# Optimization experiments

Hardware: AMD Instinct MI355X
Metric: run time of the kernel (lower is better)

## Reference

```python
import jax, jax.numpy as jnp
import numpy as np

H = 16  # num_attention_heads

def setup_inputs() -> dict:
    key = jax.random.key(0)
    ks = jax.random.split(key, 9)
    D = 1152
    def w(k, shape, scale=0.02):
        return jax.random.normal(k, shape, dtype=jnp.float32) * scale
    return {
        "hidden_states": jax.random.normal(ks[0], (16, 729, D), dtype=jnp.float32),
        "q_w": w(ks[1], (D, D)), "q_b": w(ks[2], (D,)),
        "k_w": w(ks[3], (D, D)), "k_b": w(ks[4], (D,)),
        "v_w": w(ks[5], (D, D)), "v_b": w(ks[6], (D,)),
        "o_w": w(ks[7], (D, D)), "o_b": w(ks[8], (D,)),
    }

def reference(hidden_states, q_w, q_b, k_w, k_b, v_w, v_b, o_w, o_b):
    B, S, D = hidden_states.shape
    hd = D // H
    scale = hd ** -0.5
    # projections (torch Linear: x @ W.T + b)
    q = hidden_states @ q_w.T + q_b
    k = hidden_states @ k_w.T + k_b
    v = hidden_states @ v_w.T + v_b
    # [B, H, S, hd]
    q = q.reshape(B, S, H, hd).transpose(0, 2, 1, 3)
    k = k.reshape(B, S, H, hd).transpose(0, 2, 1, 3)
    v = v.reshape(B, S, H, hd).transpose(0, 2, 1, 3)
    scores = jnp.einsum('bhqd,bhkd->bhqk', q, k) * scale
    attn = jax.nn.softmax(scores.astype(jnp.float32), axis=-1).astype(q.dtype)
    # dropout p=0.0 / eval mode -> identity
    out = jnp.einsum('bhqk,bhkd->bhqd', attn, v)  # [B,H,S,hd]
    out = out.transpose(0, 2, 1, 3).reshape(B, S, D)
    out = out @ o_w.T + o_b
    return (out, attn)
```

## Files before the change

kernel.cpp:

```cpp
#include <hip/hip_runtime.h>
#include <cstdint>
#include <cstddef>

typedef _Float16 half8 __attribute__((ext_vector_type(8)));
typedef _Float16 half4 __attribute__((ext_vector_type(4)));
typedef float    f32x4 __attribute__((ext_vector_type(4)));
typedef float    fvec4 __attribute__((ext_vector_type(4)));

#define DEV __device__ __forceinline__

constexpr int S_  = 729;
constexpr int D_  = 1152;
constexpr int H_  = 16;
constexpr int HD_ = 72;
constexpr int B_  = 16;
constexpr int M1  = B_ * S_;
constexpr int SP  = 768;
constexpr int HDP = 96;
constexpr int QSTR = 104;
constexpr float SCALE = 0.11785113019775793f;

DEV void gload16(const void* g, void* l) {
  typedef const __attribute__((address_space(1))) unsigned int GU;
  typedef __attribute__((address_space(3))) unsigned int LU;
  __builtin_amdgcn_global_load_lds((GU*)g, (LU*)l, 16, 0, 0);
}

__global__ void cvt_f32_f16(const float* __restrict__ src, _Float16* __restrict__ dst, int n4) {
  int stride = gridDim.x * blockDim.x;
  for (int i = blockIdx.x * blockDim.x + threadIdx.x; i < n4; i += stride) {
    fvec4 v = ((const fvec4*)src)[i];
    half4 o;
    o[0] = (_Float16)v[0]; o[1] = (_Float16)v[1];
    o[2] = (_Float16)v[2]; o[3] = (_Float16)v[3];
    ((half4*)dst)[i] = o;
  }
}

__global__ __launch_bounds__(256) void gemm_qkv(
    const _Float16* __restrict__ A, const _Float16* __restrict__ W,
    const float* __restrict__ qb, const float* __restrict__ kb, const float* __restrict__ vb,
    _Float16* __restrict__ q16, _Float16* __restrict__ k16, _Float16* __restrict__ vT16)
{
  __shared__ _Float16 lA[128 * 32];
  __shared__ _Float16 lB[128 * 32];
  const int tid  = threadIdx.x;
  const int wave = tid >> 6, lane = tid & 63;
  const int wr = wave >> 1, wc = wave & 1;
  const int l15 = lane & 15, l4 = lane >> 4;
  const int rowBase = blockIdx.y * 128;
  const int colBase = blockIdx.x * 128;

  f32x4 acc[4][4] = {};

  for (int kt = 0; kt < 36; ++kt) {
#pragma unroll
    for (int p = 0; p < 2; ++p) {
      int u = p * 256 + tid;
      int r = u >> 2, q = u & 3;
      int row = rowBase + r; if (row > M1 - 1) row = M1 - 1;
      gload16(A + ((size_t)row * 1152 + kt * 32 + q * 8), &lA[u * 8]);
      gload16(W + ((size_t)(colBase + r) * 1152 + kt * 32 + q * 8), &lB[u * 8]);
    }
    __syncthreads();
    half8 af[4], bf[4];
#pragma unroll
    for (int i = 0; i < 4; ++i) {
      af[i] = *(const half8*)&lA[(wr * 64 + i * 16 + l15) * 32 + l4 * 8];
      bf[i] = *(const half8*)&lB[(wc * 64 + i * 16 + l15) * 32 + l4 * 8];
    }
#pragma unroll
    for (int mi = 0; mi < 4; ++mi)
#pragma unroll
      for (int ni = 0; ni < 4; ++ni)
        acc[mi][ni] = __builtin_amdgcn_mfma_f32_16x16x32_f16(af[mi], bf[ni], acc[mi][ni], 0, 0, 0);
    __syncthreads();
  }

  const int which = colBase / 1152;
  const int wi0 = colBase - which * 1152 + wc * 64;
  const float* bias = (which == 0) ? qb : (which == 1) ? kb : vb;
#pragma unroll
  for (int ni = 0; ni < 4; ++ni) {
    int wi = wi0 + ni * 16 + l15;
    int hh = wi / 72;
    int dd = wi - hh * 72;
    float bv = bias[wi];
#pragma unroll
    for (int mi = 0; mi < 4; ++mi) {
#pragma unroll
      for (int reg = 0; reg < 4; ++reg) {
        int m = rowBase + wr * 64 + mi * 16 + l4 * 4 + reg;
        if (m < M1) {
          float val = acc[mi][ni][reg] + bv;
          int b = m / 729;
          int s = m - b * 729;
          int bh = b * 16 + hh;
          if (which == 0)      q16[((size_t)bh * SP + s) * QSTR + dd] = (_Float16)val;
          else if (which == 1) k16[((size_t)bh * SP + s) * QSTR + dd] = (_Float16)val;
          else                 vT16[((size_t)bh * HDP + dd) * SP + s] = (_Float16)val;
        }
      }
    }
  }
}

__global__ __launch_bounds__(256) void attn_fused(
    const _Float16* __restrict__ q16, const _Float16* __restrict__ k16,
    const _Float16* __restrict__ vT16,
    float* __restrict__ attnOut,
    _Float16* __restrict__ pv16)
{
  __shared__ _Float16 sQ[32 * QSTR];
  __shared__ _Float16 sK[128 * QSTR];
  __shared__ float    sS[32 * 772];
  __shared__ float    sM[32];
  __shared__ float    sL[32];

  const int tid  = threadIdx.x;
  const int wave = tid >> 6, lane = tid & 63;
  const int l15 = lane & 15, l4 = lane >> 4;
  const int rb = blockIdx.x;
  const int bh = blockIdx.y;

  const _Float16* Qg = q16 + ((size_t)bh * SP + rb * 32) * QSTR;
  const _Float16* Kg = k16 + (size_t)bh * SP * QSTR;
  const _Float16* Vg = vT16 + (size_t)bh * HDP * SP;

  for (int u = tid; u < 416; u += 256)
    gload16((const char*)Qg + u * 16, (char*)sQ + u * 16);

  for (int ct = 0; ct < 6; ++ct) {
    for (int u = tid; u < 1664; u += 256)
      gload16((const char*)Kg + (size_t)ct * 128 * QSTR * 2 + u * 16, (char*)sK + u * 16);
    __syncthreads();
    f32x4 acc[2][2] = {};
#pragma unroll
    for (int kk = 0; kk < 3; ++kk) {
      half8 a[2], bb[2];
#pragma unroll
      for (int i = 0; i < 2; ++i) {
        a[i]  = *(const half8*)&sQ[(i * 16 + l15) * QSTR + kk * 32 + l4 * 8];
        bb[i] = *(const half8*)&sK[(wave * 32 + i * 16 + l15) * QSTR + kk * 32 + l4 * 8];
      }
#pragma unroll
      for (int mi = 0; mi < 2; ++mi)
#pragma unroll
        for (int ni = 0; ni < 2; ++ni)
          acc[mi][ni] = __builtin_amdgcn_mfma_f32_16x16x32_f16(a[mi], bb[ni], acc[mi][ni], 0, 0, 0);
    }
#pragma unroll
    for (int mi = 0; mi < 2; ++mi)
#pragma unroll
      for (int ni = 0; ni < 2; ++ni)
#pragma unroll
        for (int reg = 0; reg < 4; ++reg)
          sS[(mi * 16 + l4 * 4 + reg) * 772 + ct * 128 + wave * 32 + ni * 16 + l15] =
              acc[mi][ni][reg] * SCALE;
    __syncthreads();
  }

  {
    int r = tid >> 3, j = tid & 7;
    const float* row = &sS[r * 772];
    float mx = -1e30f;
    for (int c = j; c < S_; c += 8) mx = fmaxf(mx, row[c]);
#pragma unroll
    for (int o = 1; o < 8; o <<= 1) mx = fmaxf(mx, __shfl_xor(mx, o));
    float sum = 0.f;
    for (int c = j; c < S_; c += 8) sum += __expf(row[c] - mx);
#pragma unroll
    for (int o = 1; o < 8; o <<= 1) sum += __shfl_xor(sum, o);
    if (j == 0) { sM[r] = mx; sL[r] = 1.0f / sum; }
  }
  __syncthreads();

  {
    const int wm = wave >> 1, wn = wave & 1;
    const int arow = wm * 16 + l15;
    const float mrow = sM[arow];
    const float rl = sL[arow];
    f32x4 pacc[3] = {};
    for (int kk = 0; kk < 24; ++kk) {
      const float* sp = &sS[arow * 772 + kk * 32 + l4 * 8];
      half8 a;
#pragma unroll
      for (int t = 0; t < 8; ++t) a[t] = (_Float16)(__expf(sp[t] - mrow) * rl);
#pragma unroll
      for (int f = 0; f < 3; ++f) {
        const half8 bv = *(const half8*)(Vg + (size_t)(wn * 48 + f * 16 + l15) * SP + kk * 32 + l4 * 8);
        pacc[f] = __builtin_amdgcn_mfma_f32_16x16x32_f16(a, bv, pacc[f], 0, 0, 0);
      }
    }
    const int b = bh >> 4, h = bh & 15;
#pragma unroll
    for (int f = 0; f < 3; ++f) {
      int dd = wn * 48 + f * 16 + l15;
#pragma unroll
      for (int reg = 0; reg < 4; ++reg) {
        int srow = rb * 32 + wm * 16 + l4 * 4 + reg;
        if (dd < HD_ && srow < S_)
          pv16[((size_t)(b * 729 + srow)) * 1152 + h * 72 + dd] = (_Float16)pacc[f][reg];
      }
    }
  }

  {
    float* aout = attnOut + (size_t)bh * 531441 + (size_t)rb * 32 * 729;
    int vr = S_ - rb * 32; if (vr > 32) vr = 32;
    for (int r = 0; r < vr; ++r) {
      float mx = sM[r], rl = sL[r];
      const float* row = &sS[r * 772];
      for (int c = tid; c < S_; c += 256)
        aout[(size_t)r * 729 + c] = __expf(row[c] - mx) * rl;
    }
  }
}

__global__ __launch_bounds__(256) void gemm_out(
    const _Float16* __restrict__ A, const _Float16* __restrict__ W,
    const float* __restrict__ ob, float* __restrict__ Cout)
{
  __shared__ _Float16 lA[128 * 32];
  __shared__ _Float16 lB[128 * 32];
  const int tid  = threadIdx.x;
  const int wave = tid >> 6, lane = tid & 63;
  const int wr = wave >> 1, wc = wave & 1;
  const int l15 = lane & 15, l4 = lane >> 4;
  const int rowBase = blockIdx.y * 128;
  const int colBase = blockIdx.x * 128;

  f32x4 acc[4][4] = {};

  for (int kt = 0; kt < 36; ++kt) {
#pragma unroll
    for (int p = 0; p < 2; ++p) {
      int u = p * 256 + tid;
      int r = u >> 2, q = u & 3;
      int row = rowBase + r; if (row > M1 - 1) row = M1 - 1;
      gload16(A + ((size_t)row * 1152 + kt * 32 + q * 8), &lA[u * 8]);
      gload16(W + ((size_t)(colBase + r) * 1152 + kt * 32 + q * 8), &lB[u * 8]);
    }
    __syncthreads();
    half8 af[4], bf[4];
#pragma unroll
    for (int i = 0; i < 4; ++i) {
      af[i] = *(const half8*)&lA[(wr * 64 + i * 16 + l15) * 32 + l4 * 8];
      bf[i] = *(const half8*)&lB[(wc * 64 + i * 16 + l15) * 32 + l4 * 8];
    }
#pragma unroll
    for (int mi = 0; mi < 4; ++mi)
#pragma unroll
      for (int ni = 0; ni < 4; ++ni)
        acc[mi][ni] = __builtin_amdgcn_mfma_f32_16x16x32_f16(af[mi], bf[ni], acc[mi][ni], 0, 0, 0);
    __syncthreads();
  }

#pragma unroll
  for (int ni = 0; ni < 4; ++ni) {
    int n = colBase + wc * 64 + ni * 16 + l15;
    float bv = ob[n];
#pragma unroll
    for (int mi = 0; mi < 4; ++mi) {
#pragma unroll
      for (int reg = 0; reg < 4; ++reg) {
        int m = rowBase + wr * 64 + mi * 16 + l4 * 4 + reg;
        if (m < M1) Cout[(size_t)m * 1152 + n] = acc[mi][ni][reg] + bv;
      }
    }
  }
}

extern "C" void kernel_launch(void* const* d_in, const int* in_sizes, int n_in,
                              void* d_out, int out_size, void* d_ws, size_t ws_size,
                              hipStream_t stream) {
  const float* hs = (const float*)d_in[0];
  const float* qw = (const float*)d_in[1];
  const float* qb = (const float*)d_in[2];
  const float* kw = (const float*)d_in[3];
  const float* kb = (const float*)d_in[4];
  const float* vw = (const float*)d_in[5];
  const float* vb = (const float*)d_in[6];
  const float* ow = (const float*)d_in[7];
  const float* ob = (const float*)d_in[8];

  char* ws = (char*)d_ws;
  size_t off = 0;
  auto alloc = [&](size_t bytes) {
    char* p = ws + off;
    off = (off + bytes + 255) & ~(size_t)255;
    return p;
  };
  _Float16* h16    = (_Float16*)alloc((size_t)M1 * D_ * 2);
  _Float16* wqkv16 = (_Float16*)alloc((size_t)3456 * 1152 * 2);
  _Float16* ow16   = (_Float16*)alloc((size_t)1152 * 1152 * 2);
  _Float16* q16    = (_Float16*)alloc((size_t)256 * SP * QSTR * 2);
  _Float16* k16    = (_Float16*)alloc((size_t)256 * SP * QSTR * 2);
  _Float16* vT16   = (_Float16*)alloc((size_t)256 * HDP * SP * 2);
  _Float16* pv16   = (_Float16*)alloc((size_t)M1 * D_ * 2);

  hipMemsetAsync(q16,  0, (size_t)256 * SP * QSTR * 2, stream);
  hipMemsetAsync(k16,  0, (size_t)256 * SP * QSTR * 2, stream);
  hipMemsetAsync(vT16, 0, (size_t)256 * HDP * SP * 2, stream);

  cvt_f32_f16<<<2048, 256, 0, stream>>>(hs, h16, M1 * D_ / 4);
  cvt_f32_f16<<<512, 256, 0, stream>>>(qw, wqkv16,                 1152 * 1152 / 4);
  cvt_f32_f16<<<512, 256, 0, stream>>>(kw, wqkv16 + 1152 * 1152,   1152 * 1152 / 4);
  cvt_f32_f16<<<512, 256, 0, stream>>>(vw, wqkv16 + 2 * 1152 * 1152, 1152 * 1152 / 4);
  cvt_f32_f16<<<512, 256, 0, stream>>>(ow, ow16, 1152 * 1152 / 4);

  gemm_qkv<<<dim3(27, 92), 256, 0, stream>>>(h16, wqkv16, qb, kb, vb, q16, k16, vT16);

  float* attn_out = (float*)d_out + (size_t)M1 * D_;
  attn_fused<<<dim3(23, 256), 256, 0, stream>>>(q16, k16, vT16, attn_out, pv16);

  gemm_out<<<dim3(9, 92), 256, 0, stream>>>(pv16, ow16, ob, (float*)d_out);
}
```

Before: 1.566 ms.

## Double-buffer K tiles, widen attention block to 512 threads, store exps once

The attention kernel moves to 512 threads per block and double-buffers K tiles in LDS, using manual vmcnt waits and raw barriers so the next tile's load overlaps the current QK^T MFMAs. Softmax exponentials are computed once and written back into the score buffer. The attention-probability output is written with vectorized float4 stores, and the 1/sum normalization is deferred to the PV output. The PV product is split across two K halves with an LDS reduction, and block indices are swizzled for better locality. The hand-tuned waitcnt counts and extra LDS raise the risk of correctness problems and of lower occupancy.

```diff
diff --git a/kernel.cpp b/kernel.cpp
--- a/kernel.cpp
+++ b/kernel.cpp
@@ -5,6 +5,7 @@
 typedef _Float16 half8 __attribute__((ext_vector_type(8)));
 typedef _Float16 half4 __attribute__((ext_vector_type(4)));
 typedef float    f32x4 __attribute__((ext_vector_type(4)));
+typedef float    f32x4_u __attribute__((ext_vector_type(4), aligned(4)));
 typedef float    fvec4 __attribute__((ext_vector_type(4)));
 
 #define DEV __device__ __forceinline__
@@ -25,6 +26,8 @@
   typedef __attribute__((address_space(3))) unsigned int LU;
   __builtin_amdgcn_global_load_lds((GU*)g, (LU*)l, 16, 0, 0);
 }
+
+DEV void fence_mem() { asm volatile("" ::: "memory"); }
 
 __global__ void cvt_f32_f16(const float* __restrict__ src, _Float16* __restrict__ dst, int n4) {
   int stride = gridDim.x * blockDim.x;
@@ -105,114 +108,150 @@
   }
 }
 
-__global__ __launch_bounds__(256) void attn_fused(
+DEV void stageK(const _Float16* src, _Float16* dst, int wv, int lane) {
+  for (int c = wv; c < 26; c += 8)
+    gload16((const char*)src + c * 1024 + lane * 16, (char*)dst + c * 1024 + lane * 16);
+}
+
+__global__ __launch_bounds__(512) void attn_fused(
     const _Float16* __restrict__ q16, const _Float16* __restrict__ k16,
     const _Float16* __restrict__ vT16,
     float* __restrict__ attnOut,
     _Float16* __restrict__ pv16)
 {
-  __shared__ _Float16 sQ[32 * QSTR];
-  __shared__ _Float16 sK[128 * QSTR];
-  __shared__ float    sS[32 * 772];
-  __shared__ float    sM[32];
-  __shared__ float    sL[32];
+  __shared__ __align__(16) _Float16 sQ[32 * QSTR];
+  __shared__ __align__(16) _Float16 sKb[2][128 * QSTR];
+  __shared__ __align__(16) float    sS[32 * 772];
+  __shared__ float sL[32];
+  float* red = (float*)&sKb[0][0];
 
   const int tid  = threadIdx.x;
-  const int wave = tid >> 6, lane = tid & 63;
-  const int l15 = lane & 15, l4 = lane >> 4;
-  const int rb = blockIdx.x;
-  const int bh = blockIdx.y;
+  const int wv   = tid >> 6, lane = tid & 63;
+  const int l15  = lane & 15, l4 = lane >> 4;
+
+  const int lin  = blockIdx.y * 23 + blockIdx.x;
+  const int nlin = (lin & 7) * 736 + (lin >> 3);
+  const int bh   = nlin / 23;
+  const int rb   = nlin - bh * 23;
 
   const _Float16* Qg = q16 + ((size_t)bh * SP + rb * 32) * QSTR;
   const _Float16* Kg = k16 + (size_t)bh * SP * QSTR;
   const _Float16* Vg = vT16 + (size_t)bh * HDP * SP;
 
-  for (int u = tid; u < 416; u += 256)
-    gload16((const char*)Qg + u * 16, (char*)sQ + u * 16);
+  if (tid < 416) {
+    half8 v = *(const half8*)(Qg + tid * 8);
+    *(half8*)(sQ + tid * 8) = v;
+  }
+  stageK(Kg, sKb[0], wv, lane);
+  __syncthreads();
 
   for (int ct = 0; ct < 6; ++ct) {
-    for (int u = tid; u < 1664; u += 256)
-      gload16((const char*)Kg + (size_t)ct * 128 * QSTR * 2 + u * 16, (char*)sK + u * 16);
-    __syncthreads();
-    f32x4 acc[2][2] = {};
+    const _Float16* cur = sKb[ct & 1];
+    if (ct < 5) {
+      stageK(Kg + (ct + 1) * (128 * QSTR), sKb[(ct + 1) & 1], wv, lane);
+      if (wv < 2) asm volatile("s_waitcnt vmcnt(4)" ::: "memory");
+      else        asm volatile("s_waitcnt vmcnt(3)" ::: "memory");
+    } else {
+      asm volatile("s_waitcnt vmcnt(0)" ::: "memory");
+    }
+    __builtin_amdgcn_s_barrier();
+    fence_mem();
+
+    f32x4 acc0 = {0.f, 0.f, 0.f, 0.f};
+    f32x4 acc1 = {0.f, 0.f, 0.f, 0.f};
 #pragma unroll
     for (int kk = 0; kk < 3; ++kk) {
-      half8 a[2], bb[2];
-#pragma unroll
-      for (int i = 0; i < 2; ++i) {
-        a[i]  = *(const half8*)&sQ[(i * 16 + l15) * QSTR + kk * 32 + l4 * 8];
-        bb[i] = *(const half8*)&sK[(wave * 32 + i * 16 + l15) * QSTR + kk * 32 + l4 * 8];
+      half8 a0 = *(const half8*)&sQ[(l15) * QSTR + kk * 32 + l4 * 8];
+      half8 a1 = *(const half8*)&sQ[(16 + l15) * QSTR + kk * 32 + l4 * 8];
+      half8 b  = *(const half8*)&cur[(wv * 16 + l15) * QSTR + kk * 32 + l4 * 8];
+      acc0 = __builtin_amdgcn_mfma_f32_16x16x32_f16(a0, b, acc0, 0, 0, 0);
+      acc1 = __builtin_amdgcn_mfma_f32_16x16x32_f16(a1, b, acc1, 0, 0, 0);
+    }
+#pragma unroll
+    for (int r = 0; r < 4; ++r) {
+      sS[(l4 * 4 + r) * 772 + ct * 128 + wv * 16 + l15]        = acc0[r] * SCALE;
+      sS[(16 + l4 * 4 + r) * 772 + ct * 128 + wv * 16 + l15]   = acc1[r] * SCALE;
+    }
+    asm volatile("s_waitcnt lgkmcnt(0)" ::: "memory");
+    __builtin_amdgcn_s_barrier();
+    fence_mem();
+  }
+
+  const int sr = tid >> 4, sj = tid & 15;
+  float m = -1e30f;
+  for (int c = sj; c < 729; c += 16) m = fmaxf(m, sS[sr * 772 + c]);
+#pragma unroll
+  for (int o = 1; o < 16; o <<= 1) m = fmaxf(m, __shfl_xor(m, o));
+  float sum = 0.f;
+  for (int c = sj; c < 768; c += 16) {
+    float s = sS[sr * 772 + c];
+    float e = (c < 729) ? __expf(s - m) : 0.f;
+    sS[sr * 772 + c] = e;
+    sum += e;
+  }
+#pragma unroll
+  for (int o = 1; o < 16; o <<= 1) sum += __shfl_xor(sum, o);
+  const float rl = 1.0f / sum;
+  if (sj == 0) sL[sr] = rl;
+  __syncthreads();
+
+  {
+    const int grow = rb * 32 + sr;
+    float* aout = attnOut + (size_t)bh * 531441 + (size_t)grow * 729;
+    if (grow < 729) {
+#pragma unroll
+      for (int it = 0; it < 12; ++it) {
+        int c4 = sj + it * 16;
+        if (c4 < 182) {
+          f32x4 e = *(const f32x4*)&sS[sr * 772 + c4 * 4];
+          f32x4 p = e * rl;
+          *(f32x4_u*)&aout[c4 * 4] = p;
+        }
       }
-#pragma unroll
-      for (int mi = 0; mi < 2; ++mi)
-#pragma unroll
-        for (int ni = 0; ni < 2; ++ni)
-          acc[mi][ni] = __builtin_amdgcn_mfma_f32_16x16x32_f16(a[mi], bb[ni], acc[mi][ni], 0, 0, 0);
-    }
-#pragma unroll
-    for (int mi = 0; mi < 2; ++mi)
-#pragma unroll
-      for (int ni = 0; ni < 2; ++ni)
-#pragma unroll
-        for (int reg = 0; reg < 4; ++reg)
-          sS[(mi * 16 + l4 * 4 + reg) * 772 + ct * 128 + wave * 32 + ni * 16 + l15] =
-              acc[mi][ni][reg] * SCALE;
-    __syncthreads();
-  }
-
-  {
-    int r = tid >> 3, j = tid & 7;
-    const float* row = &sS[r * 772];
-    float mx = -1e30f;
-    for (int c = j; c < S_; c += 8) mx = fmaxf(mx, row[c]);
-#pragma unroll
-    for (int o = 1; o < 8; o <<= 1) mx = fmaxf(mx, __shfl_xor(mx, o));
-    float sum = 0.f;
-    for (int c = j; c < S_; c += 8) sum += __expf(row[c] - mx);
-#pragma unroll
-    for (int o = 1; o < 8; o <<= 1) sum += __shfl_xor(sum, o);
-    if (j == 0) { sM[r] = mx; sL[r] = 1.0f / sum; }
+      if (sj == 6) aout[728] = sS[sr * 772 + 728] * rl;
+    }
+  }
+
+  const int wm = wv >> 2, wn = (wv >> 1) & 1, kh = wv & 1;
+  f32x4 pacc[3] = {};
+  const _Float16* Vw = Vg + (size_t)wn * 48 * SP;
+  for (int kk = kh * 12; kk < kh * 12 + 12; ++kk) {
+    const float* sp = &sS[(wm * 16 + l15) * 772 + kk * 32 + l4 * 8];
+    f32x4 e0 = *(const f32x4*)sp;
+    f32x4 e1 = *(const f32x4*)(sp + 4);
+    half8 a;
+    a[0] = (_Float16)e0[0]; a[1] = (_Float16)e0[1];
+    a[2] = (_Float16)e0[2]; a[3] = (_Float16)e0[3];
+    a[4] = (_Float16)e1[0]; a[5] = (_Float16)e1[1];
+    a[6] = (_Float16)e1[2]; a[7] = (_Float16)e1[3];
+#pragma unroll
+    for (int f = 0; f < 3; ++f) {
+      half8 bv = *(const half8*)&Vw[(size_t)(f * 16 + l15) * SP + kk * 32 + l4 * 8];
+      pacc[f] = __builtin_amdgcn_mfma_f32_16x16x32_f16(a, bv, pacc[f], 0, 0, 0);
+    }
+  }
+  const int unit = wv >> 1;
+  if (kh == 1) {
+#pragma unroll
+    for (int f = 0; f < 3; ++f)
+      *(f32x4*)&red[((unit * 3 + f) * 64 + lane) * 4] = pacc[f];
   }
   __syncthreads();
-
-  {
-    const int wm = wave >> 1, wn = wave & 1;
-    const int arow = wm * 16 + l15;
-    const float mrow = sM[arow];
-    const float rl = sL[arow];
-    f32x4 pacc[3] = {};
-    for (int kk = 0; kk < 24; ++kk) {
-      const float* sp = &sS[arow * 772 + kk * 32 + l4 * 8];
-      half8 a;
-#pragma unroll
-      for (int t = 0; t < 8; ++t) a[t] = (_Float16)(__expf(sp[t] - mrow) * rl);
-#pragma unroll
-      for (int f = 0; f < 3; ++f) {
-        const half8 bv = *(const half8*)(Vg + (size_t)(wn * 48 + f * 16 + l15) * SP + kk * 32 + l4 * 8);
-        pacc[f] = __builtin_amdgcn_mfma_f32_16x16x32_f16(a, bv, pacc[f], 0, 0, 0);
+  if (kh == 0) {
+    const int b = bh >> 4, h = bh & 15;
+#pragma unroll
+    for (int f = 0; f < 3; ++f) {
+      f32x4 o = pacc[f] + *(const f32x4*)&red[((unit * 3 + f) * 64 + lane) * 4];
+      int dd = wn * 48 + f * 16 + l15;
+#pragma unroll
+      for (int r = 0; r < 4; ++r) {
+        int row  = wm * 16 + l4 * 4 + r;
+        int srow = rb * 32 + row;
+        if (dd < HD_ && srow < S_) {
+          float val = o[r] * sL[row];
+          pv16[((size_t)(b * 729 + srow)) * 1152 + h * 72 + dd] = (_Float16)val;
+        }
       }
-    }
-    const int b = bh >> 4, h = bh & 15;
-#pragma unroll
-    for (int f = 0; f < 3; ++f) {
-      int dd = wn * 48 + f * 16 + l15;
-#pragma unroll
-      for (int reg = 0; reg < 4; ++reg) {
-        int srow = rb * 32 + wm * 16 + l4 * 4 + reg;
-        if (dd < HD_ && srow < S_)
-          pv16[((size_t)(b * 729 + srow)) * 1152 + h * 72 + dd] = (_Float16)pacc[f][reg];
-      }
-    }
-  }
-
-  {
-    float* aout = attnOut + (size_t)bh * 531441 + (size_t)rb * 32 * 729;
-    int vr = S_ - rb * 32; if (vr > 32) vr = 32;
-    for (int r = 0; r < vr; ++r) {
-      float mx = sM[r], rl = sL[r];
-      const float* row = &sS[r * 772];
-      for (int c = tid; c < S_; c += 256)
-        aout[(size_t)r * 729 + c] = __expf(row[c] - mx) * rl;
     }
   }
 }
@@ -304,15 +343,15 @@
   hipMemsetAsync(vT16, 0, (size_t)256 * HDP * SP * 2, stream);
 
   cvt_f32_f16<<<2048, 256, 0, stream>>>(hs, h16, M1 * D_ / 4);
-  cvt_f32_f16<<<512, 256, 0, stream>>>(qw, wqkv16,                 1152 * 1152 / 4);
-  cvt_f32_f16<<<512, 256, 0, stream>>>(kw, wqkv16 + 1152 * 1152,   1152 * 1152 / 4);
+  cvt_f32_f16<<<512, 256, 0, stream>>>(qw, wqkv16,                   1152 * 1152 / 4);
+  cvt_f32_f16<<<512, 256, 0, stream>>>(kw, wqkv16 + 1152 * 1152,     1152 * 1152 / 4);
   cvt_f32_f16<<<512, 256, 0, stream>>>(vw, wqkv16 + 2 * 1152 * 1152, 1152 * 1152 / 4);
   cvt_f32_f16<<<512, 256, 0, stream>>>(ow, ow16, 1152 * 1152 / 4);
 
   gemm_qkv<<<dim3(27, 92), 256, 0, stream>>>(h16, wqkv16, qb, kb, vb, q16, k16, vT16);
 
   float* attn_out = (float*)d_out + (size_t)M1 * D_;
-  attn_fused<<<dim3(23, 256), 256, 0, stream>>>(q16, k16, vT16, attn_out, pv16);
+  attn_fused<<<dim3(23, 256), 512, 0, stream>>>(q16, k16, vT16, attn_out, pv16);
 
   gemm_out<<<dim3(9, 92), 256, 0, stream>>>(pv16, ow16, ob, (float*)d_out);
 }
```

New measurement: 1.373 ms. 12.3% less time.

## Rewrite attention kernel to keep scores in registers with split-K softmax

Applied to the files above, without the earlier changes.

The attention kernel now processes 16 query rows per block. Each of the four waves owns a 192-key slice and keeps its scores in registers, so the large LDS score buffer is gone. Per-wave max and sum statistics are combined through a small LDS exchange, probabilities are written straight to the attention output with vector stores, and the PV products from each wave are reduced through LDS. A swizzled block index and launch bounds aimed at higher occupancy are added. In exchange it relies on heavy register use for the score tiles, switches to the smaller 16x16x16 MFMA for PV, and leaves the final normalization to the end.

```diff
diff --git a/kernel.cpp b/kernel.cpp
--- a/kernel.cpp
+++ b/kernel.cpp
@@ -5,6 +5,7 @@
 typedef _Float16 half8 __attribute__((ext_vector_type(8)));
 typedef _Float16 half4 __attribute__((ext_vector_type(4)));
 typedef float    f32x4 __attribute__((ext_vector_type(4)));
+typedef float    f32x4_u __attribute__((ext_vector_type(4), aligned(4)));
 typedef float    fvec4 __attribute__((ext_vector_type(4)));
 
 #define DEV __device__ __forceinline__
@@ -105,114 +106,131 @@
   }
 }
 
-__global__ __launch_bounds__(256) void attn_fused(
+__global__ __launch_bounds__(256, 4) void attn_fused(
     const _Float16* __restrict__ q16, const _Float16* __restrict__ k16,
     const _Float16* __restrict__ vT16,
     float* __restrict__ attnOut,
     _Float16* __restrict__ pv16)
 {
-  __shared__ _Float16 sQ[32 * QSTR];
-  __shared__ _Float16 sK[128 * QSTR];
-  __shared__ float    sS[32 * 772];
-  __shared__ float    sM[32];
-  __shared__ float    sL[32];
+  __shared__ __align__(16) float sRed[3][16][80];
+  __shared__ float sStat[4][16][2];
 
   const int tid  = threadIdx.x;
-  const int wave = tid >> 6, lane = tid & 63;
-  const int l15 = lane & 15, l4 = lane >> 4;
-  const int rb = blockIdx.x;
-  const int bh = blockIdx.y;
-
-  const _Float16* Qg = q16 + ((size_t)bh * SP + rb * 32) * QSTR;
-  const _Float16* Kg = k16 + (size_t)bh * SP * QSTR;
-  const _Float16* Vg = vT16 + (size_t)bh * HDP * SP;
-
-  for (int u = tid; u < 416; u += 256)
-    gload16((const char*)Qg + u * 16, (char*)sQ + u * 16);
-
-  for (int ct = 0; ct < 6; ++ct) {
-    for (int u = tid; u < 1664; u += 256)
-      gload16((const char*)Kg + (size_t)ct * 128 * QSTR * 2 + u * 16, (char*)sK + u * 16);
-    __syncthreads();
-    f32x4 acc[2][2] = {};
-#pragma unroll
-    for (int kk = 0; kk < 3; ++kk) {
-      half8 a[2], bb[2];
-#pragma unroll
-      for (int i = 0; i < 2; ++i) {
-        a[i]  = *(const half8*)&sQ[(i * 16 + l15) * QSTR + kk * 32 + l4 * 8];
-        bb[i] = *(const half8*)&sK[(wave * 32 + i * 16 + l15) * QSTR + kk * 32 + l4 * 8];
+  const int wv   = tid >> 6, lane = tid & 63;
+  const int l15  = lane & 15, l4 = lane >> 4;
+
+  const int lin  = blockIdx.y * 48 + blockIdx.x;
+  const int nlin = (lin & 7) * 1536 + (lin >> 3);
+  const int bh   = nlin / 48;
+  const int rb   = nlin - bh * 48;
+  const int q0   = rb * 16;
+
+  const _Float16* Qg = q16 + ((size_t)bh * SP + q0) * QSTR;
+  const _Float16* Kg = k16 + ((size_t)bh * SP + wv * 192) * QSTR;
+  const _Float16* Vg = vT16 + (size_t)bh * HDP * SP + wv * 192;
+
+  half8 qf[3];
+#pragma unroll
+  for (int d = 0; d < 3; ++d)
+    qf[d] = *(const half8*)(Qg + (size_t)l15 * QSTR + d * 32 + l4 * 8);
+
+  float sc[12][4];
+  float m_ln = -1e30f;
+#pragma unroll
+  for (int t = 0; t < 12; ++t) {
+    f32x4 a = {0.f, 0.f, 0.f, 0.f};
+#pragma unroll
+    for (int d = 0; d < 3; ++d) {
+      half8 kf = *(const half8*)(Kg + (size_t)(t * 16 + l15) * QSTR + d * 32 + l4 * 8);
+      a = __builtin_amdgcn_mfma_f32_16x16x32_f16(kf, qf[d], a, 0, 0, 0);
+    }
+#pragma unroll
+    for (int r = 0; r < 4; ++r) {
+      int kidx = wv * 192 + t * 16 + l4 * 4 + r;
+      float s = (kidx < S_) ? a[r] * SCALE : -1e30f;
+      sc[t][r] = s;
+      m_ln = fmaxf(m_ln, s);
+    }
+  }
+  float l_ln = 0.f;
+#pragma unroll
+  for (int t = 0; t < 12; ++t)
+#pragma unroll
+    for (int r = 0; r < 4; ++r) l_ln += __expf(sc[t][r] - m_ln);
+
+#pragma unroll
+  for (int o = 16; o < 64; o <<= 1) {
+    float mo = __shfl_xor(m_ln, o), lo = __shfl_xor(l_ln, o);
+    float M2 = fmaxf(m_ln, mo);
+    l_ln = l_ln * __expf(m_ln - M2) + lo * __expf(mo - M2);
+    m_ln = M2;
+  }
+  if (lane < 16) { sStat[wv][l15][0] = m_ln; sStat[wv][l15][1] = l_ln; }
+  __syncthreads();
+
+  float M = sStat[0][l15][0], L = sStat[0][l15][1];
+#pragma unroll
+  for (int k = 1; k < 4; ++k) {
+    float mk = sStat[k][l15][0], lk = sStat[k][l15][1];
+    float Mn = fmaxf(M, mk);
+    L = L * __expf(M - Mn) + lk * __expf(mk - Mn);
+    M = Mn;
+  }
+  const float rl = 1.0f / L;
+
+  const bool qvalid = (q0 + l15) < S_;
+  float* arow = attnOut + (size_t)bh * 531441 + (size_t)(q0 + l15) * 729;
+
+  f32x4 pacc[5] = {};
+#pragma unroll
+  for (int t = 0; t < 12; ++t) {
+    int kbase = wv * 192 + t * 16 + l4 * 4;
+    f32x4 e;
+#pragma unroll
+    for (int r = 0; r < 4; ++r) e[r] = __expf(sc[t][r] - M);
+
+    if (qvalid) {
+      if (kbase + 3 < S_) {
+        f32x4 p = e * rl;
+        *(f32x4_u*)(arow + kbase) = p;
+      } else {
+#pragma unroll
+        for (int r = 0; r < 4; ++r)
+          if (kbase + r < S_) arow[kbase + r] = e[r] * rl;
       }
-#pragma unroll
-      for (int mi = 0; mi < 2; ++mi)
-#pragma unroll
-        for (int ni = 0; ni < 2; ++ni)
-          acc[mi][ni] = __builtin_amdgcn_mfma_f32_16x16x32_f16(a[mi], bb[ni], acc[mi][ni], 0, 0, 0);
-    }
-#pragma unroll
-    for (int mi = 0; mi < 2; ++mi)
-#pragma unroll
-      for (int ni = 0; ni < 2; ++ni)
-#pragma unroll
-        for (int reg = 0; reg < 4; ++reg)
-          sS[(mi * 16 + l4 * 4 + reg) * 772 + ct * 128 + wave * 32 + ni * 16 + l15] =
-              acc[mi][ni][reg] * SCALE;
-    __syncthreads();
-  }
-
-  {
-    int r = tid >> 3, j = tid & 7;
-    const float* row = &sS[r * 772];
-    float mx = -1e30f;
-    for (int c = j; c < S_; c += 8) mx = fmaxf(mx, row[c]);
-#pragma unroll
-    for (int o = 1; o < 8; o <<= 1) mx = fmaxf(mx, __shfl_xor(mx, o));
-    float sum = 0.f;
-    for (int c = j; c < S_; c += 8) sum += __expf(row[c] - mx);
-#pragma unroll
-    for (int o = 1; o < 8; o <<= 1) sum += __shfl_xor(sum, o);
-    if (j == 0) { sM[r] = mx; sL[r] = 1.0f / sum; }
+    }
+
+    half4 pb;
+#pragma unroll
+    for (int r = 0; r < 4; ++r) pb[r] = (_Float16)e[r];
+#pragma unroll
+    for (int dt = 0; dt < 5; ++dt) {
+      half4 vf = *(const half4*)(Vg + (size_t)(dt * 16 + l15) * SP + t * 16 + l4 * 4);
+      pacc[dt] = __builtin_amdgcn_mfma_f32_16x16x16f16(vf, pb, pacc[dt], 0, 0, 0);
+    }
+  }
+
+  if (wv > 0) {
+#pragma unroll
+    for (int dt = 0; dt < 5; ++dt)
+      *(f32x4*)&sRed[wv - 1][l15][dt * 16 + l4 * 4] = pacc[dt];
   }
   __syncthreads();
-
-  {
-    const int wm = wave >> 1, wn = wave & 1;
-    const int arow = wm * 16 + l15;
-    const float mrow = sM[arow];
-    const float rl = sL[arow];
-    f32x4 pacc[3] = {};
-    for (int kk = 0; kk < 24; ++kk) {
-      const float* sp = &sS[arow * 772 + kk * 32 + l4 * 8];
-      half8 a;
-#pragma unroll
-      for (int t = 0; t < 8; ++t) a[t] = (_Float16)(__expf(sp[t] - mrow) * rl);
-#pragma unroll
-      for (int f = 0; f < 3; ++f) {
-        const half8 bv = *(const half8*)(Vg + (size_t)(wn * 48 + f * 16 + l15) * SP + kk * 32 + l4 * 8);
-        pacc[f] = __builtin_amdgcn_mfma_f32_16x16x32_f16(a, bv, pacc[f], 0, 0, 0);
+  if (wv == 0) {
+    const int b = bh >> 4, h = bh & 15;
+#pragma unroll
+    for (int dt = 0; dt < 5; ++dt) {
+      f32x4 o = pacc[dt];
+#pragma unroll
+      for (int w = 0; w < 3; ++w)
+        o += *(const f32x4*)&sRed[w][l15][dt * 16 + l4 * 4];
+      int dbase = dt * 16 + l4 * 4;
+      if (qvalid && dbase < HD_) {
+        half4 ov;
+#pragma unroll
+        for (int r = 0; r < 4; ++r) ov[r] = (_Float16)(o[r] * rl);
+        *(half4*)(pv16 + (size_t)(b * 729 + q0 + l15) * 1152 + h * 72 + dbase) = ov;
       }
-    }
-    const int b = bh >> 4, h = bh & 15;
-#pragma unroll
-    for (int f = 0; f < 3; ++f) {
-      int dd = wn * 48 + f * 16 + l15;
-#pragma unroll
-      for (int reg = 0; reg < 4; ++reg) {
-        int srow = rb * 32 + wm * 16 + l4 * 4 + reg;
-        if (dd < HD_ && srow < S_)
-          pv16[((size_t)(b * 729 + srow)) * 1152 + h * 72 + dd] = (_Float16)pacc[f][reg];
-      }
-    }
-  }
-
-  {
-    float* aout = attnOut + (size_t)bh * 531441 + (size_t)rb * 32 * 729;
-    int vr = S_ - rb * 32; if (vr > 32) vr = 32;
-    for (int r = 0; r < vr; ++r) {
-      float mx = sM[r], rl = sL[r];
-      const float* row = &sS[r * 772];
-      for (int c = tid; c < S_; c += 256)
-        aout[(size_t)r * 729 + c] = __expf(row[c] - mx) * rl;
     }
   }
 }
@@ -299,20 +317,20 @@
   _Float16* vT16   = (_Float16*)alloc((size_t)256 * HDP * SP * 2);
   _Float16* pv16   = (_Float16*)alloc((size_t)M1 * D_ * 2);
 
-  hipMemsetAsync(q16,  0, (size_t)256 * SP * QSTR * 2, stream);
-  hipMemsetAsync(k16,  0, (size_t)256 * SP * QSTR * 2, stream);
-  hipMemsetAsync(vT16, 0, (size_t)256 * HDP * SP * 2, stream);
+  (void)hipMemsetAsync(q16,  0, (size_t)256 * SP * QSTR * 2, stream);
+  (void)hipMemsetAsync(k16,  0, (size_t)256 * SP * QSTR * 2, stream);
+  (void)hipMemsetAsync(vT16, 0, (size_t)256 * HDP * SP * 2, stream);
 
   cvt_f32_f16<<<2048, 256, 0, stream>>>(hs, h16, M1 * D_ / 4);
-  cvt_f32_f16<<<512, 256, 0, stream>>>(qw, wqkv16,                 1152 * 1152 / 4);
-  cvt_f32_f16<<<512, 256, 0, stream>>>(kw, wqkv16 + 1152 * 1152,   1152 * 1152 / 4);
+  cvt_f32_f16<<<512, 256, 0, stream>>>(qw, wqkv16,                   1152 * 1152 / 4);
+  cvt_f32_f16<<<512, 256, 0, stream>>>(kw, wqkv16 + 1152 * 1152,     1152 * 1152 / 4);
   cvt_f32_f16<<<512, 256, 0, stream>>>(vw, wqkv16 + 2 * 1152 * 1152, 1152 * 1152 / 4);
   cvt_f32_f16<<<512, 256, 0, stream>>>(ow, ow16, 1152 * 1152 / 4);
 
   gemm_qkv<<<dim3(27, 92), 256, 0, stream>>>(h16, wqkv16, qb, kb, vb, q16, k16, vT16);
 
   float* attn_out = (float*)d_out + (size_t)M1 * D_;
-  attn_fused<<<dim3(23, 256), 256, 0, stream>>>(q16, k16, vT16, attn_out, pv16);
+  attn_fused<<<dim3(48, 256), 256, 0, stream>>>(q16, k16, vT16, attn_out, pv16);
 
   gemm_out<<<dim3(9, 92), 256, 0, stream>>>(pv16, ow16, ob, (float*)d_out);
 }
```

Measured after the change: 1.338 ms. 14.6% less time.
